# Performance work log

Hardware: AMD Instinct MI355X
Metric: run time of the kernel (lower is better)

## Reference

```python
import jax, jax.numpy as jnp
import numpy as np

B, H, S, D1, D2 = 1, 8, 4096, 64, 64


def setup_inputs() -> dict:
    key = jax.random.key(0)
    ks = jax.random.split(key, 6)
    q = jax.random.normal(ks[0], (B, H, S, D1), dtype=jnp.float32)
    k = jax.random.normal(ks[1], (B, H, S, D1), dtype=jnp.float32)
    v = jax.random.normal(ks[2], (B, H, S, D2), dtype=jnp.float32)
    # Decay coefficients per head/position (positive, like RetNet gamma^i masks)
    coef_q = jax.random.uniform(ks[3], (H, S), dtype=jnp.float32)
    coef_k = jax.random.uniform(ks[4], (H, S), dtype=jnp.float32)
    # Normalizer must be bounded away from 0
    mask_normer = jax.random.uniform(ks[5], (H, S), dtype=jnp.float32) + 0.5
    return {"q": q, "k": k, "v": v, "coef_q": coef_q, "coef_k": coef_k,
            "mask_normer": mask_normer}


def _rmsenorm(x):
    return x * jax.lax.rsqrt(jnp.mean(x * x, axis=-1, keepdims=True) + 1e-6)


def reference(q, k, v, coef_q, coef_k, mask_normer):
    # q,k: [B,H,S,D1]; v: [B,H,S,D2]; coef_*/mask_normer: [H,S]
    q_bar = q * (coef_q / mask_normer)[None, :, :, None]      # [B,H,S,D1]
    k_bar = k * coef_k[None, :, :, None]                       # [B,H,S,D1]
    # running normalization P_i = |q_i . sum_{j<=i} k_j|, clamped at 1
    T = jnp.cumsum(k_bar, axis=-2)                             # [B,H,S,D1]
    P = jnp.einsum('bhid,bhid->bhi', T, q_bar)                 # [B,H,S]
    P = jnp.maximum(jnp.abs(jax.lax.stop_gradient(P)), 1.0)[..., None]
    q_bar = q_bar / P
    # outer-product state and prefix sum over sequence
    D = jnp.einsum('bhia,bhic->bhiac', k_bar, v)               # [B,H,S,D1,D2]
    D = jnp.cumsum(D, axis=-3)                                 # cumsum over S
    O = jnp.einsum('bhia,bhiac->bhic', q_bar, D)               # [B,H,S,D2]
    return _rmsenorm(O)
```

## Files before the change

### kernel.cpp

```cpp
#include <hip/hip_runtime.h>

#define H 8
#define S 4096
#define D 64
#define C 64
#define NC (S / C)
#define PITCH 72

typedef short bf16x8 __attribute__((ext_vector_type(8)));
typedef float f32x4 __attribute__((ext_vector_type(4)));
typedef unsigned uint4v __attribute__((ext_vector_type(4)));

struct alignas(16) F4 { float v[4]; };

__device__ inline unsigned short rne_bf16(float x) {
  unsigned u = __builtin_bit_cast(unsigned, x);
  unsigned r = u + 0x7fffu + ((u >> 16) & 1u);
  return (unsigned short)(r >> 16);
}
__device__ inline float bf16_to_f(unsigned hw) {
  return __builtin_bit_cast(float, hw << 16);
}

__global__ __launch_bounds__(256) void k_chunk_sums(
    const float* __restrict__ k, const float* __restrict__ v,
    const float* __restrict__ coef_k, unsigned short* __restrict__ wsKV) {
  const int ch = blockIdx.x, h = blockIdx.y, t = threadIdx.x;
  __shared__ alignas(16) short kT[D * PITCH];
  __shared__ alignas(16) short vT[D * PITCH];

  const float* kp = k + (size_t)(h * S + ch * C) * D;
  const float* vp = v + (size_t)(h * S + ch * C) * D;
  const float* ck = coef_k + h * S + ch * C;

  const int w = t >> 6, col = t & 63;
  {
    const int i0 = (w & 1) * 32;
    const bool isK = (w < 2);
    const float* src = isK ? kp : vp;
    short* dstT = isK ? kT : vT;
    unsigned pr[16];
#pragma unroll
    for (int u2 = 0; u2 < 16; ++u2) {
      float x0 = src[(i0 + 2 * u2) * D + col];
      float x1 = src[(i0 + 2 * u2 + 1) * D + col];
      if (isK) { x0 *= ck[i0 + 2 * u2]; x1 *= ck[i0 + 2 * u2 + 1]; }
      pr[u2] = (unsigned)rne_bf16(x0) | ((unsigned)rne_bf16(x1) << 16);
    }
#pragma unroll
    for (int g = 0; g < 4; ++g) {
      uint4v wv = {pr[4 * g], pr[4 * g + 1], pr[4 * g + 2], pr[4 * g + 3]};
      *reinterpret_cast<uint4v*>(&dstT[col * PITCH + i0 + 8 * g]) = wv;
    }
  }
  __syncthreads();

  const int lane = t & 63;
  const int arow = lane & 15, kg = lane >> 4;
  const int abase = (16 * w + arow) * PITCH + 8 * kg;
  bf16x8 a0 = *reinterpret_cast<const bf16x8*>(&vT[abase]);
  bf16x8 a1 = *reinterpret_cast<const bf16x8*>(&vT[abase + 32]);
  unsigned short* dst = wsKV + (size_t)(h * NC + ch) * (D * D);
#pragma unroll
  for (int n = 0; n < 4; ++n) {
    const int bb = (16 * n + arow) * PITCH + 8 * kg;
    bf16x8 b0 = *reinterpret_cast<const bf16x8*>(&kT[bb]);
    bf16x8 b1 = *reinterpret_cast<const bf16x8*>(&kT[bb + 32]);
    f32x4 z = {0.f, 0.f, 0.f, 0.f};
    z = __builtin_amdgcn_mfma_f32_16x16x32_bf16(a0, b0, z, 0, 0, 0);
    z = __builtin_amdgcn_mfma_f32_16x16x32_bf16(a1, b1, z, 0, 0, 0);
#pragma unroll
    for (int r = 0; r < 4; ++r)
      dst[(16 * w + 4 * kg + r) * D + 16 * n + arow] = rne_bf16(z[r]);
  }
}

__global__ __launch_bounds__(64) void k_scan(unsigned* __restrict__ wsKV) {
  const int seg = blockIdx.x, h = blockIdx.y, t = threadIdx.x;
  const int e0 = seg * 64 + t;
  float run0 = 0.f, run1 = 0.f;
  for (int base = 0; base < NC; base += 32) {
    unsigned x[32];
#pragma unroll
    for (int u = 0; u < 32; ++u)
      x[u] = wsKV[(size_t)(h * NC + base + u) * 2048 + e0];
#pragma unroll
    for (int u = 0; u < 32; ++u) {
      wsKV[(size_t)(h * NC + base + u) * 2048 + e0] =
          (unsigned)rne_bf16(run0) | ((unsigned)rne_bf16(run1) << 16);
      run0 += bf16_to_f(x[u] & 0xffffu);
      run1 += bf16_to_f(x[u] >> 16);
    }
  }
}

__global__ __launch_bounds__(256) void k_chunk_out(
    const float* __restrict__ q, const float* __restrict__ k,
    const float* __restrict__ v,
    const float* __restrict__ coef_q, const float* __restrict__ coef_k,
    const float* __restrict__ mask_normer,
    const unsigned short* __restrict__ wsKV, float* __restrict__ out) {
  const int ch = blockIdx.x, h = blockIdx.y, t = threadIdx.x;
  __shared__ alignas(16) short qb[C * PITCH];
  __shared__ alignas(16) short kbf[C * PITCH];
  __shared__ alignas(16) short s0b[D * PITCH];
  __shared__ alignas(16) short vT[D * PITCH];
  __shared__ alignas(16) short Ab[C * PITCH];

  const size_t base = (size_t)(h * S + ch * C) * D;
  const float* qp = q + base;
  const float* kp = k + base;
  const float* vp = v + base;
  const float* cq = coef_q + h * S + ch * C;
  const float* ck = coef_k + h * S + ch * C;
  const float* mn = mask_normer + h * S + ch * C;
  const unsigned short* s0p = wsKV + (size_t)(h * NC + ch) * (D * D);

  {
    const int i = t >> 2, c0 = (t & 3) * 16;
    const float sq = cq[i] / mn[i];
    const float sk = ck[i];
#pragma unroll
    for (int g = 0; g < 2; ++g) {
      bf16x8 wq, wk;
#pragma unroll
      for (int u0 = 0; u0 < 8; u0 += 4) {
        F4 qv = *reinterpret_cast<const F4*>(qp + i * D + c0 + 8 * g + u0);
        F4 kv = *reinterpret_cast<const F4*>(kp + i * D + c0 + 8 * g + u0);
#pragma unroll
        for (int u = 0; u < 4; ++u) {
          wq[u0 + u] = (short)rne_bf16(qv.v[u] * sq);
          wk[u0 + u] = (short)rne_bf16(kv.v[u] * sk);
        }
      }
      *reinterpret_cast<bf16x8*>(&qb[i * PITCH + c0 + 8 * g]) = wq;
      *reinterpret_cast<bf16x8*>(&kbf[i * PITCH + c0 + 8 * g]) = wk;
      bf16x8 ws = *reinterpret_cast<const bf16x8*>(s0p + i * D + c0 + 8 * g);
      *reinterpret_cast<bf16x8*>(&s0b[i * PITCH + c0 + 8 * g]) = ws;
    }
  }
  {
    const int c = t & 63, i0 = 16 * (t >> 6);
    unsigned pr[8];
#pragma unroll
    for (int u2 = 0; u2 < 8; ++u2) {
      float x0 = vp[(size_t)(i0 + 2 * u2) * D + c];
      float x1 = vp[(size_t)(i0 + 2 * u2 + 1) * D + c];
      pr[u2] = (unsigned)rne_bf16(x0) | ((unsigned)rne_bf16(x1) << 16);
    }
#pragma unroll
    for (int g = 0; g < 2; ++g) {
      uint4v wv = {pr[4 * g], pr[4 * g + 1], pr[4 * g + 2], pr[4 * g + 3]};
      *reinterpret_cast<uint4v*>(&vT[c * PITCH + i0 + 8 * g]) = wv;
    }
  }
  __syncthreads();

  const int lane = t & 63, w = t >> 6;
  const int arow = lane & 15, kg = lane >> 4;
  const int rbase = (16 * w + arow) * PITCH + 8 * kg;

  bf16x8 qa0 = *reinterpret_cast<const bf16x8*>(&qb[rbase]);
  bf16x8 qa1 = *reinterpret_cast<const bf16x8*>(&qb[rbase + 32]);

  {
    f32x4 accA[4];
#pragma unroll
    for (int n = 0; n < 4; ++n) {
      const int bb = (16 * n + arow) * PITCH + 8 * kg;
      bf16x8 b0 = *reinterpret_cast<const bf16x8*>(&kbf[bb]);
      bf16x8 b1 = *reinterpret_cast<const bf16x8*>(&kbf[bb + 32]);
      f32x4 z = {0.f, 0.f, 0.f, 0.f};
      z = __builtin_amdgcn_mfma_f32_16x16x32_bf16(qa0, b0, z, 0, 0, 0);
      z = __builtin_amdgcn_mfma_f32_16x16x32_bf16(qa1, b1, z, 0, 0, 0);
      accA[n] = z;
    }
#pragma unroll
    for (int n = 0; n < 4; ++n)
#pragma unroll
      for (int r = 0; r < 4; ++r) {
        int i = 4 * kg + r;
        int j = 16 * n + arow;
        float x = (j <= 16 * w + i) ? accA[n][r] : 0.f;
        Ab[(16 * w + i) * PITCH + j] = (short)rne_bf16(x);
      }
  }

  bf16x8 aa0 = *reinterpret_cast<const bf16x8*>(&Ab[rbase]);
  bf16x8 aa1 = *reinterpret_cast<const bf16x8*>(&Ab[rbase + 32]);
  f32x4 accO[4];
#pragma unroll
  for (int n = 0; n < 4; ++n) {
    const int bb = (16 * n + arow) * PITCH + 8 * kg;
    bf16x8 h0 = *reinterpret_cast<const bf16x8*>(&s0b[bb]);
    bf16x8 h1 = *reinterpret_cast<const bf16x8*>(&s0b[bb + 32]);
    bf16x8 v0 = *reinterpret_cast<const bf16x8*>(&vT[bb]);
    bf16x8 v1 = *reinterpret_cast<const bf16x8*>(&vT[bb + 32]);
    f32x4 z = {0.f, 0.f, 0.f, 0.f};
    z = __builtin_amdgcn_mfma_f32_16x16x32_bf16(qa0, h0, z, 0, 0, 0);
    z = __builtin_amdgcn_mfma_f32_16x16x32_bf16(qa1, h1, z, 0, 0, 0);
    z = __builtin_amdgcn_mfma_f32_16x16x32_bf16(aa0, v0, z, 0, 0, 0);
    z = __builtin_amdgcn_mfma_f32_16x16x32_bf16(aa1, v1, z, 0, 0, 0);
    accO[n] = z;
  }

  float* op = out + base;
#pragma unroll
  for (int r = 0; r < 4; ++r) {
    const int i = 16 * w + 4 * kg + r;
    float ss = 0.f;
#pragma unroll
    for (int n = 0; n < 4; ++n) ss += accO[n][r] * accO[n][r];
#pragma unroll
    for (int off = 1; off < 16; off <<= 1) ss += __shfl_xor(ss, off);
    const float sc = rsqrtf(ss * (1.0f / D) + 1e-6f);
#pragma unroll
    for (int n = 0; n < 4; ++n)
      op[(size_t)i * D + 16 * n + arow] = accO[n][r] * sc;
  }
}

extern "C" void kernel_launch(void* const* d_in, const int* in_sizes, int n_in,
                              void* d_out, int out_size, void* d_ws, size_t ws_size,
                              hipStream_t stream) {
  (void)in_sizes; (void)n_in; (void)out_size; (void)ws_size;
  const float* q  = (const float*)d_in[0];
  const float* k  = (const float*)d_in[1];
  const float* v  = (const float*)d_in[2];
  const float* cq = (const float*)d_in[3];
  const float* ck = (const float*)d_in[4];
  const float* mn = (const float*)d_in[5];
  float* out = (float*)d_out;

  unsigned short* wsKV = (unsigned short*)d_ws;

  k_chunk_sums<<<dim3(NC, H), dim3(256), 0, stream>>>(k, v, ck, wsKV);
  k_scan<<<dim3(32, H), dim3(64), 0, stream>>>((unsigned*)d_ws);
  k_chunk_out<<<dim3(NC, H), dim3(256), 0, stream>>>(q, k, v, cq, ck, mn, wsKV, out);
}
```

Baseline: 25.69 us.

## Split chunk kernels across eight waves and read state directly from global

Both chunk kernels now launch 512 threads per block, with each wave computing half of the 16-row output tile columns, to raise wave count and latency hiding on a small grid. The output kernel no longer stages the prefix state in LDS and loads MFMA operands from global memory directly. The RMS norm reduction is split across two waves via a small shared buffer. This adds extra barriers and uncoalesced-ish global state reads.

```diff
diff --git a/kernel.cpp b/kernel.cpp
--- a/kernel.cpp
+++ b/kernel.cpp
@@ -5,6 +5,7 @@
 #define D 64
 #define C 64
 #define NC (S / C)
+#define DD (D * D)
 #define PITCH 72
 
 typedef short bf16x8 __attribute__((ext_vector_type(8)));
@@ -22,47 +23,50 @@
   return __builtin_bit_cast(float, hw << 16);
 }
 
-__global__ __launch_bounds__(256) void k_chunk_sums(
+__global__ __launch_bounds__(512, 2) void k_chunk_sums(
     const float* __restrict__ k, const float* __restrict__ v,
     const float* __restrict__ coef_k, unsigned short* __restrict__ wsKV) {
   const int ch = blockIdx.x, h = blockIdx.y, t = threadIdx.x;
-  __shared__ alignas(16) short kT[D * PITCH];
-  __shared__ alignas(16) short vT[D * PITCH];
+  __shared__ alignas(16) short kT[C * PITCH];
+  __shared__ alignas(16) short vT[C * PITCH];
 
   const float* kp = k + (size_t)(h * S + ch * C) * D;
   const float* vp = v + (size_t)(h * S + ch * C) * D;
   const float* ck = coef_k + h * S + ch * C;
 
-  const int w = t >> 6, col = t & 63;
   {
-    const int i0 = (w & 1) * 32;
-    const bool isK = (w < 2);
+    const int col = t & 63, grp = t >> 6;
+    const bool isK = grp < 4;
+    const int i0 = (grp & 3) * 16;
     const float* src = isK ? kp : vp;
     short* dstT = isK ? kT : vT;
-    unsigned pr[16];
-#pragma unroll
-    for (int u2 = 0; u2 < 16; ++u2) {
-      float x0 = src[(i0 + 2 * u2) * D + col];
-      float x1 = src[(i0 + 2 * u2 + 1) * D + col];
-      if (isK) { x0 *= ck[i0 + 2 * u2]; x1 *= ck[i0 + 2 * u2 + 1]; }
+    unsigned pr[8];
+#pragma unroll
+    for (int u2 = 0; u2 < 8; ++u2) {
+      const int ia = i0 + 2 * u2, ib = ia + 1;
+      float x0 = src[ia * D + col];
+      float x1 = src[ib * D + col];
+      if (isK) { x0 *= ck[ia]; x1 *= ck[ib]; }
       pr[u2] = (unsigned)rne_bf16(x0) | ((unsigned)rne_bf16(x1) << 16);
     }
 #pragma unroll
-    for (int g = 0; g < 4; ++g) {
+    for (int g = 0; g < 2; ++g) {
       uint4v wv = {pr[4 * g], pr[4 * g + 1], pr[4 * g + 2], pr[4 * g + 3]};
       *reinterpret_cast<uint4v*>(&dstT[col * PITCH + i0 + 8 * g]) = wv;
     }
   }
   __syncthreads();
 
-  const int lane = t & 63;
+  const int lane = t & 63, w = t >> 6;
   const int arow = lane & 15, kg = lane >> 4;
-  const int abase = (16 * w + arow) * PITCH + 8 * kg;
+  const int m = w >> 1, n0 = 2 * (w & 1);
+  const int abase = (16 * m + arow) * PITCH + 8 * kg;
   bf16x8 a0 = *reinterpret_cast<const bf16x8*>(&vT[abase]);
   bf16x8 a1 = *reinterpret_cast<const bf16x8*>(&vT[abase + 32]);
-  unsigned short* dst = wsKV + (size_t)(h * NC + ch) * (D * D);
-#pragma unroll
-  for (int n = 0; n < 4; ++n) {
+  unsigned short* dst = wsKV + (size_t)(h * NC + ch) * DD;
+#pragma unroll
+  for (int nn = 0; nn < 2; ++nn) {
+    const int n = n0 + nn;
     const int bb = (16 * n + arow) * PITCH + 8 * kg;
     bf16x8 b0 = *reinterpret_cast<const bf16x8*>(&kT[bb]);
     bf16x8 b1 = *reinterpret_cast<const bf16x8*>(&kT[bb + 32]);
@@ -71,7 +75,7 @@
     z = __builtin_amdgcn_mfma_f32_16x16x32_bf16(a1, b1, z, 0, 0, 0);
 #pragma unroll
     for (int r = 0; r < 4; ++r)
-      dst[(16 * w + 4 * kg + r) * D + 16 * n + arow] = rne_bf16(z[r]);
+      dst[(16 * m + 4 * kg + r) * D + 16 * n + arow] = rne_bf16(z[r]);
   }
 }
 
@@ -94,7 +98,7 @@
   }
 }
 
-__global__ __launch_bounds__(256) void k_chunk_out(
+__global__ __launch_bounds__(512, 2) void k_chunk_out(
     const float* __restrict__ q, const float* __restrict__ k,
     const float* __restrict__ v,
     const float* __restrict__ coef_q, const float* __restrict__ coef_k,
@@ -103,9 +107,9 @@
   const int ch = blockIdx.x, h = blockIdx.y, t = threadIdx.x;
   __shared__ alignas(16) short qb[C * PITCH];
   __shared__ alignas(16) short kbf[C * PITCH];
-  __shared__ alignas(16) short s0b[D * PITCH];
-  __shared__ alignas(16) short vT[D * PITCH];
+  __shared__ alignas(16) short vT[C * PITCH];
   __shared__ alignas(16) short Ab[C * PITCH];
+  __shared__ float ssp[C][2];
 
   const size_t base = (size_t)(h * S + ch * C) * D;
   const float* qp = q + base;
@@ -114,86 +118,77 @@
   const float* cq = coef_q + h * S + ch * C;
   const float* ck = coef_k + h * S + ch * C;
   const float* mn = mask_normer + h * S + ch * C;
-  const unsigned short* s0p = wsKV + (size_t)(h * NC + ch) * (D * D);
+  const unsigned short* s0p = wsKV + (size_t)(h * NC + ch) * DD;
 
   {
-    const int i = t >> 2, c0 = (t & 3) * 16;
+    const int i = t >> 3, c0 = (t & 7) * 8;
     const float sq = cq[i] / mn[i];
     const float sk = ck[i];
-#pragma unroll
-    for (int g = 0; g < 2; ++g) {
-      bf16x8 wq, wk;
-#pragma unroll
-      for (int u0 = 0; u0 < 8; u0 += 4) {
-        F4 qv = *reinterpret_cast<const F4*>(qp + i * D + c0 + 8 * g + u0);
-        F4 kv = *reinterpret_cast<const F4*>(kp + i * D + c0 + 8 * g + u0);
-#pragma unroll
-        for (int u = 0; u < 4; ++u) {
-          wq[u0 + u] = (short)rne_bf16(qv.v[u] * sq);
-          wk[u0 + u] = (short)rne_bf16(kv.v[u] * sk);
-        }
+    bf16x8 wq, wk;
+#pragma unroll
+    for (int u0 = 0; u0 < 8; u0 += 4) {
+      F4 qv = *reinterpret_cast<const F4*>(qp + i * D + c0 + u0);
+      F4 kv = *reinterpret_cast<const F4*>(kp + i * D + c0 + u0);
+#pragma unroll
+      for (int u = 0; u < 4; ++u) {
+        wq[u0 + u] = (short)rne_bf16(qv.v[u] * sq);
+        wk[u0 + u] = (short)rne_bf16(kv.v[u] * sk);
       }
-      *reinterpret_cast<bf16x8*>(&qb[i * PITCH + c0 + 8 * g]) = wq;
-      *reinterpret_cast<bf16x8*>(&kbf[i * PITCH + c0 + 8 * g]) = wk;
-      bf16x8 ws = *reinterpret_cast<const bf16x8*>(s0p + i * D + c0 + 8 * g);
-      *reinterpret_cast<bf16x8*>(&s0b[i * PITCH + c0 + 8 * g]) = ws;
-    }
+    }
+    *reinterpret_cast<bf16x8*>(&qb[i * PITCH + c0]) = wq;
+    *reinterpret_cast<bf16x8*>(&kbf[i * PITCH + c0]) = wk;
   }
   {
-    const int c = t & 63, i0 = 16 * (t >> 6);
-    unsigned pr[8];
-#pragma unroll
-    for (int u2 = 0; u2 < 8; ++u2) {
-      float x0 = vp[(size_t)(i0 + 2 * u2) * D + c];
-      float x1 = vp[(size_t)(i0 + 2 * u2 + 1) * D + c];
+    const int col = t & 63, i0 = 8 * (t >> 6);
+    unsigned pr[4];
+#pragma unroll
+    for (int u2 = 0; u2 < 4; ++u2) {
+      float x0 = vp[(size_t)(i0 + 2 * u2) * D + col];
+      float x1 = vp[(size_t)(i0 + 2 * u2 + 1) * D + col];
       pr[u2] = (unsigned)rne_bf16(x0) | ((unsigned)rne_bf16(x1) << 16);
     }
-#pragma unroll
-    for (int g = 0; g < 2; ++g) {
-      uint4v wv = {pr[4 * g], pr[4 * g + 1], pr[4 * g + 2], pr[4 * g + 3]};
-      *reinterpret_cast<uint4v*>(&vT[c * PITCH + i0 + 8 * g]) = wv;
-    }
+    uint4v wv = {pr[0], pr[1], pr[2], pr[3]};
+    *reinterpret_cast<uint4v*>(&vT[col * PITCH + i0]) = wv;
   }
   __syncthreads();
 
   const int lane = t & 63, w = t >> 6;
   const int arow = lane & 15, kg = lane >> 4;
-  const int rbase = (16 * w + arow) * PITCH + 8 * kg;
+  const int m = w >> 1, n0 = 2 * (w & 1);
+  const int rbase = (16 * m + arow) * PITCH + 8 * kg;
 
   bf16x8 qa0 = *reinterpret_cast<const bf16x8*>(&qb[rbase]);
   bf16x8 qa1 = *reinterpret_cast<const bf16x8*>(&qb[rbase + 32]);
 
-  {
-    f32x4 accA[4];
-#pragma unroll
-    for (int n = 0; n < 4; ++n) {
-      const int bb = (16 * n + arow) * PITCH + 8 * kg;
-      bf16x8 b0 = *reinterpret_cast<const bf16x8*>(&kbf[bb]);
-      bf16x8 b1 = *reinterpret_cast<const bf16x8*>(&kbf[bb + 32]);
-      f32x4 z = {0.f, 0.f, 0.f, 0.f};
-      z = __builtin_amdgcn_mfma_f32_16x16x32_bf16(qa0, b0, z, 0, 0, 0);
-      z = __builtin_amdgcn_mfma_f32_16x16x32_bf16(qa1, b1, z, 0, 0, 0);
-      accA[n] = z;
-    }
-#pragma unroll
-    for (int n = 0; n < 4; ++n)
-#pragma unroll
-      for (int r = 0; r < 4; ++r) {
-        int i = 4 * kg + r;
-        int j = 16 * n + arow;
-        float x = (j <= 16 * w + i) ? accA[n][r] : 0.f;
-        Ab[(16 * w + i) * PITCH + j] = (short)rne_bf16(x);
-      }
-  }
+#pragma unroll
+  for (int nn = 0; nn < 2; ++nn) {
+    const int n = n0 + nn;
+    const int bb = (16 * n + arow) * PITCH + 8 * kg;
+    bf16x8 b0 = *reinterpret_cast<const bf16x8*>(&kbf[bb]);
+    bf16x8 b1 = *reinterpret_cast<const bf16x8*>(&kbf[bb + 32]);
+    f32x4 z = {0.f, 0.f, 0.f, 0.f};
+    z = __builtin_amdgcn_mfma_f32_16x16x32_bf16(qa0, b0, z, 0, 0, 0);
+    z = __builtin_amdgcn_mfma_f32_16x16x32_bf16(qa1, b1, z, 0, 0, 0);
+#pragma unroll
+    for (int r = 0; r < 4; ++r) {
+      int i = 16 * m + 4 * kg + r;
+      int j = 16 * n + arow;
+      float x = (j <= i) ? z[r] : 0.f;
+      Ab[i * PITCH + j] = (short)rne_bf16(x);
+    }
+  }
+  __syncthreads();
 
   bf16x8 aa0 = *reinterpret_cast<const bf16x8*>(&Ab[rbase]);
   bf16x8 aa1 = *reinterpret_cast<const bf16x8*>(&Ab[rbase + 32]);
-  f32x4 accO[4];
-#pragma unroll
-  for (int n = 0; n < 4; ++n) {
+  f32x4 accO[2];
+#pragma unroll
+  for (int nn = 0; nn < 2; ++nn) {
+    const int n = n0 + nn;
     const int bb = (16 * n + arow) * PITCH + 8 * kg;
-    bf16x8 h0 = *reinterpret_cast<const bf16x8*>(&s0b[bb]);
-    bf16x8 h1 = *reinterpret_cast<const bf16x8*>(&s0b[bb + 32]);
+    const int gb = (16 * n + arow) * D + 8 * kg;
+    bf16x8 h0 = *reinterpret_cast<const bf16x8*>(s0p + gb);
+    bf16x8 h1 = *reinterpret_cast<const bf16x8*>(s0p + gb + 32);
     bf16x8 v0 = *reinterpret_cast<const bf16x8*>(&vT[bb]);
     bf16x8 v1 = *reinterpret_cast<const bf16x8*>(&vT[bb + 32]);
     f32x4 z = {0.f, 0.f, 0.f, 0.f};
@@ -201,22 +196,27 @@
     z = __builtin_amdgcn_mfma_f32_16x16x32_bf16(qa1, h1, z, 0, 0, 0);
     z = __builtin_amdgcn_mfma_f32_16x16x32_bf16(aa0, v0, z, 0, 0, 0);
     z = __builtin_amdgcn_mfma_f32_16x16x32_bf16(aa1, v1, z, 0, 0, 0);
-    accO[n] = z;
-  }
+    accO[nn] = z;
+  }
+
+#pragma unroll
+  for (int r = 0; r < 4; ++r) {
+    float ss = accO[0][r] * accO[0][r] + accO[1][r] * accO[1][r];
+#pragma unroll
+    for (int off = 1; off < 16; off <<= 1) ss += __shfl_xor(ss, off);
+    if (arow == 0) ssp[16 * m + 4 * kg + r][w & 1] = ss;
+  }
+  __syncthreads();
 
   float* op = out + base;
 #pragma unroll
   for (int r = 0; r < 4; ++r) {
-    const int i = 16 * w + 4 * kg + r;
-    float ss = 0.f;
-#pragma unroll
-    for (int n = 0; n < 4; ++n) ss += accO[n][r] * accO[n][r];
-#pragma unroll
-    for (int off = 1; off < 16; off <<= 1) ss += __shfl_xor(ss, off);
-    const float sc = rsqrtf(ss * (1.0f / D) + 1e-6f);
-#pragma unroll
-    for (int n = 0; n < 4; ++n)
-      op[(size_t)i * D + 16 * n + arow] = accO[n][r] * sc;
+    const int i = 16 * m + 4 * kg + r;
+    const float tot = ssp[i][0] + ssp[i][1];
+    const float sc = rsqrtf(tot * (1.0f / D) + 1e-6f);
+#pragma unroll
+    for (int nn = 0; nn < 2; ++nn)
+      op[(size_t)i * D + 16 * (n0 + nn) + arow] = accO[nn][r] * sc;
   }
 }
 
@@ -234,7 +234,7 @@
 
   unsigned short* wsKV = (unsigned short*)d_ws;
 
-  k_chunk_sums<<<dim3(NC, H), dim3(256), 0, stream>>>(k, v, ck, wsKV);
+  k_chunk_sums<<<dim3(NC, H), dim3(512), 0, stream>>>(k, v, ck, wsKV);
   k_scan<<<dim3(32, H), dim3(64), 0, stream>>>((unsigned*)d_ws);
-  k_chunk_out<<<dim3(NC, H), dim3(256), 0, stream>>>(q, k, v, cq, ck, mn, wsKV, out);
-}
+  k_chunk_out<<<dim3(NC, H), dim3(512), 0, stream>>>(q, k, v, cq, ck, mn, wsKV, out);
+}
```

Measured after the change: 24.15 us, median of 2. 6.0% less time.
